# Optimization experiments

Measured on AMD Instinct MI355X. Metric: run time of the kernel, lower is better.

## Reference

```python
import math
import jax, jax.numpy as jnp
import numpy as np

CHANNELS = 256
NUM_HEADS = 4
GROUPS = 32
EPS = 1e-5


def setup_inputs() -> dict:
    key = jax.random.key(0)
    ks = jax.random.split(key, 7)
    b, c, h, w = 8, CHANNELS, 48, 48
    return {
        "x": jax.random.normal(ks[0], (b, c, h, w), dtype=jnp.float32),
        "gn_w": jax.random.uniform(ks[1], (c,), dtype=jnp.float32),
        "gn_b": jax.random.normal(ks[2], (c,), dtype=jnp.float32) * 0.02,
        "qkv_w": jax.random.normal(ks[3], (3 * c, c), dtype=jnp.float32) * (1.0 / math.sqrt(c)),
        "qkv_b": jax.random.normal(ks[4], (3 * c,), dtype=jnp.float32) * 0.02,
        "proj_w": jax.random.normal(ks[5], (c, c), dtype=jnp.float32) * (1.0 / math.sqrt(c)),
        "proj_b": jax.random.normal(ks[6], (c,), dtype=jnp.float32) * 0.02,
    }


def reference(x, gn_w, gn_b, qkv_w, qkv_b, proj_w, proj_b):
    b, c, h, w = x.shape
    nh = NUM_HEADS
    hd = c // nh
    hw = h * w

    # GroupNorm(32, c): normalize over (c/G, h, w) per group
    xg = x.reshape(b, GROUPS, c // GROUPS, h, w)
    mean = jnp.mean(xg, axis=(2, 3, 4), keepdims=True)
    var = jnp.mean(jnp.square(xg - mean), axis=(2, 3, 4), keepdims=True)
    xn = (xg - mean) * jax.lax.rsqrt(var + EPS)
    xn = xn.reshape(b, c, h, w) * gn_w[None, :, None, None] + gn_b[None, :, None, None]

    # 1x1 conv qkv: per-pixel linear
    qkv = jnp.einsum('bchw,oc->bohw', xn, qkv_w) + qkv_b[None, :, None, None]
    q, k, v = jnp.split(qkv, 3, axis=1)  # each (b, c, h, w)

    # split channels into heads: (b, nh, hd, hw)
    q = q.reshape(b, nh, hd, hw)
    k = k.reshape(b, nh, hd, hw)
    v = v.reshape(b, nh, hd, hw)

    scale = 1.0 / math.sqrt(hd)
    attn = jnp.einsum('bndi,bndj->bnij', q, k) * scale  # (b, nh, hw, hw)
    attn = jax.nn.softmax(attn, axis=-1)
    out = jnp.einsum('bnij,bndj->bndi', attn, v)  # (b, nh, hd, hw)
    out = out.reshape(b, c, h, w)

    out = jnp.einsum('bchw,oc->bohw', out, proj_w) + proj_b[None, :, None, None]
    return x + out
```

## Files before the change

kernel.cpp:

```cpp
#include <hip/hip_runtime.h>
#include <hip/hip_bf16.h>
#include <math.h>

#define NB 8
#define NC 256
#define NHW 2304
#define NH 4
#define HD 64
#define CPG 8
#define GN_EPS 1e-5f

typedef __bf16 bf16;
typedef __bf16 bf16x4 __attribute__((ext_vector_type(4)));
typedef __bf16 bf16x8 __attribute__((ext_vector_type(8)));
typedef float f32x4 __attribute__((ext_vector_type(4)));
typedef float f32x16 __attribute__((ext_vector_type(16)));
typedef int i32x4 __attribute__((ext_vector_type(4)));
typedef unsigned int u32;

#define MFMA16(a, b, c) __builtin_amdgcn_mfma_f32_16x16x32_bf16(a, b, c, 0, 0, 0)
#define MFMA32(a, b, c) __builtin_amdgcn_mfma_f32_32x32x16_bf16(a, b, c, 0, 0, 0)

__global__ __launch_bounds__(256) void k_pre(const float* __restrict__ x,
                                             const float* __restrict__ gw,
                                             const float* __restrict__ gb,
                                             const float* __restrict__ qw,
                                             const float* __restrict__ pw,
                                             bf16* __restrict__ xnt,
                                             bf16* __restrict__ wq,
                                             bf16* __restrict__ wp) {
  int t = threadIdx.x;
  if (blockIdx.x < 768) {
    int i = blockIdx.x * 256 + t;
    wq[i] = (bf16)qw[i];
    if (i < NC * NC) wp[i] = (bf16)pw[i];
    return;
  }
  int bid = blockIdx.x - 768;
  int b = bid >> 5;
  int g = bid & 31;
  int c0 = g * CPG;
  const float* xb = x + (b * NC + c0) * NHW;
  float s = 0.f, s2 = 0.f;
  for (int p = t; p < NHW; p += 256) {
#pragma unroll
    for (int cc = 0; cc < CPG; ++cc) {
      float v = xb[cc * NHW + p];
      s += v;
      s2 += v * v;
    }
  }
#pragma unroll
  for (int m = 1; m < 64; m <<= 1) {
    s += __shfl_xor(s, m);
    s2 += __shfl_xor(s2, m);
  }
  __shared__ float red[8];
  int wid = t >> 6;
  if ((t & 63) == 0) { red[wid] = s; red[4 + wid] = s2; }
  __syncthreads();
  s = red[0] + red[1] + red[2] + red[3];
  s2 = red[4] + red[5] + red[6] + red[7];
  const float inv_n = 1.0f / (CPG * NHW);
  float mean = s * inv_n;
  float var = s2 * inv_n - mean * mean;
  float rsq = rsqrtf(var + GN_EPS);
  float ka[CPG], kb[CPG];
#pragma unroll
  for (int cc = 0; cc < CPG; ++cc) {
    float wv = gw[c0 + cc];
    ka[cc] = wv * rsq;
    kb[cc] = gb[c0 + cc] - mean * rsq * wv;
  }
  bf16* dst = xnt + b * NHW * NC + c0;
  for (int p = t; p < NHW; p += 256) {
    bf16x8 o;
#pragma unroll
    for (int cc = 0; cc < CPG; ++cc)
      o[cc] = (bf16)(xb[cc * NHW + p] * ka[cc] + kb[cc]);
    *reinterpret_cast<bf16x8*>(dst + p * NC) = o;
  }
}

__global__ __launch_bounds__(256) void k_qkv(const bf16* __restrict__ xnt,
                                             const bf16* __restrict__ wq,
                                             const float* __restrict__ qkvb,
                                             bf16* __restrict__ qt,
                                             bf16* __restrict__ kt,
                                             bf16* __restrict__ vv) {
  int b = blockIdx.z;
  int i_base = blockIdx.x * 128;
  int o_base = blockIdx.y * 128;
  int t = threadIdx.x;
  int lane = t & 63, wid = t >> 6;
  int wm = (wid >> 1) * 64, wn = (wid & 1) * 64;
  int l15 = lane & 15, g = lane >> 4;
  const bool qk = (o_base < 512);
  const bf16* ab;
  const bf16* bb;
  if (qk) {
    ab = wq + (o_base + wm + l15) * NC + g * 8;
    bb = xnt + ((size_t)b * NHW + i_base + wn + l15) * NC + g * 8;
  } else {
    ab = xnt + ((size_t)b * NHW + i_base + wm + l15) * NC + g * 8;
    bb = wq + (o_base + wn + l15) * NC + g * 8;
  }
  f32x4 acc[4][4] = {};
#pragma unroll 2
  for (int kc = 0; kc < 8; ++kc) {
    bf16x8 af[4], bf[4];
#pragma unroll
    for (int mf = 0; mf < 4; ++mf)
      af[mf] = *reinterpret_cast<const bf16x8*>(ab + mf * 16 * NC + kc * 32);
#pragma unroll
    for (int nf = 0; nf < 4; ++nf)
      bf[nf] = *reinterpret_cast<const bf16x8*>(bb + nf * 16 * NC + kc * 32);
#pragma unroll
    for (int mf = 0; mf < 4; ++mf)
#pragma unroll
      for (int nf = 0; nf < 4; ++nf)
        acc[mf][nf] = MFMA16(af[mf], bf[nf], acc[mf][nf]);
  }
  if (qk) {
    const float qscale = 0.125f * 1.4426950408889634f;
#pragma unroll
    for (int mf = 0; mf < 4; ++mf) {
      int o0 = o_base + wm + mf * 16 + g * 4;
      f32x4 b4 = *reinterpret_cast<const f32x4*>(qkvb + o0);
      bool isQ = (o0 < 256);
      float sc = isQ ? qscale : 1.0f;
      int oo = isQ ? o0 : o0 - 256;
      bf16* base = (isQ ? qt : kt) +
                   ((size_t)(b * NH + (oo >> 6)) * NHW) * HD + (oo & 63);
#pragma unroll
      for (int nf = 0; nf < 4; ++nf) {
        int i = i_base + wn + nf * 16 + l15;
        bf16x4 w;
#pragma unroll
        for (int r = 0; r < 4; ++r)
          w[r] = (bf16)((acc[mf][nf][r] + b4[r]) * sc);
        *reinterpret_cast<bf16x4*>(base + (size_t)i * HD) = w;
      }
    }
  } else {
#pragma unroll
    for (int nf = 0; nf < 4; ++nf) {
      int og = o_base + wn + nf * 16 + l15;
      float bias = qkvb[og];
      int o2 = og - 512;
      bf16* dp = vv + ((size_t)(b * NH + (o2 >> 6)) * HD + (o2 & 63)) * NHW +
                 i_base + wm + g * 4;
#pragma unroll
      for (int mf = 0; mf < 4; ++mf) {
        bf16x4 w;
#pragma unroll
        for (int r = 0; r < 4; ++r) w[r] = (bf16)(acc[mf][nf][r] + bias);
        *reinterpret_cast<bf16x4*>(dp + mf * 16) = w;
      }
    }
  }
}

__global__ __launch_bounds__(256, 4) void k_attn(const bf16* __restrict__ qt,
                                                 const bf16* __restrict__ kt,
                                                 const bf16* __restrict__ vv,
                                                 bf16* __restrict__ att) {
  __shared__ union SM {
    struct { bf16 k[2][4096]; bf16 v[2][4096]; } kv;
    float m[2][64][33];
  } smem;

  const int tid = threadIdx.x;
  const int wid = tid >> 6, lane = tid & 63;
  const int l31 = lane & 31, g2 = lane >> 5;
  const int ig = wid & 1, jsub = wid >> 1;

  const int bid = blockIdx.x;
  const int wg = (bid & 7) * 144 + (bid >> 3);
  const int bh = wg / 36, it = wg % 36;
  const int b = bh >> 2, n = bh & 3;
  const int i0w = it * 64 + ig * 32;

  const bf16* qb = qt + (size_t)bh * NHW * HD;
  const bf16* kb = kt + (size_t)bh * NHW * HD;
  const bf16* vb = vv + (size_t)bh * HD * NHW;

  const int r0 = tid >> 3, cs = tid & 7;
  const bf16* kg0 = kb + r0 * HD + cs * 8;
  const bf16* kg1 = kb + (r0 + 32) * HD + cs * 8;
  const bf16* vg0 = vb + (size_t)r0 * NHW + cs * 8;
  const bf16* vg1 = vb + (size_t)(r0 + 32) * NHW + cs * 8;
#define EOFF(c, row) ((c) * 512 + ((((row) + (c)) & 63) << 3))
  const int lw0 = EOFF(cs, r0);
  const int lw1 = EOFF(cs, r0 + 32);

  int ksw[4];
#pragma unroll
  for (int kk = 0; kk < 4; ++kk) ksw[kk] = EOFF(2 * kk + g2, jsub * 32 + l31);
  int vsw0[2], vsw1[2];
#pragma unroll
  for (int J = 0; J < 2; ++J) {
    int c = jsub * 4 + J * 2 + g2;
    vsw0[J] = EOFF(c, l31);
    vsw1[J] = EOFF(c, l31 + 32);
  }
#undef EOFF

  bf16x8 q[4];
#pragma unroll
  for (int kk = 0; kk < 4; ++kk)
    q[kk] = *reinterpret_cast<const bf16x8*>(qb + (i0w + l31) * HD + kk * 16 + g2 * 8);

  f32x16 acc0 = {}, acc1 = {};
  float l_r = 0.f;

  {
    bf16x8 a = *reinterpret_cast<const bf16x8*>(kg0);
    bf16x8 c = *reinterpret_cast<const bf16x8*>(kg1);
    bf16x8 d = *reinterpret_cast<const bf16x8*>(vg0);
    bf16x8 e = *reinterpret_cast<const bf16x8*>(vg1);
    *reinterpret_cast<bf16x8*>(&smem.kv.k[0][lw0]) = a;
    *reinterpret_cast<bf16x8*>(&smem.kv.k[0][lw1]) = c;
    *reinterpret_cast<bf16x8*>(&smem.kv.v[0][lw0]) = d;
    *reinterpret_cast<bf16x8*>(&smem.kv.v[0][lw1]) = e;
  }
  asm volatile("s_waitcnt lgkmcnt(0)" ::: "memory");
  __builtin_amdgcn_s_barrier();

  for (int t = 0; t < 36; ++t) {
    const int cur = t & 1;
    bf16x8 kr0, kr1, vr0, vr1;
    if (t < 35) {
      kr0 = *reinterpret_cast<const bf16x8*>(kg0 + (t + 1) * (64 * HD));
      kr1 = *reinterpret_cast<const bf16x8*>(kg1 + (t + 1) * (64 * HD));
      vr0 = *reinterpret_cast<const bf16x8*>(vg0 + (t + 1) * 64);
      vr1 = *reinterpret_cast<const bf16x8*>(vg1 + (t + 1) * 64);
    }
    const bf16* kc = smem.kv.k[cur];
    const bf16* vc = smem.kv.v[cur];

    f32x16 s = {};
    __builtin_amdgcn_s_setprio(1);
#pragma unroll
    for (int kk = 0; kk < 4; ++kk) {
      bf16x8 kf = *reinterpret_cast<const bf16x8*>(kc + ksw[kk]);
      s = MFMA32(kf, q[kk], s);
    }
    __builtin_amdgcn_s_setprio(0);

    u32 P[8];
    float la = 0.f, lb = 0.f;
#pragma unroll
    for (int m = 0; m < 8; ++m) {
      float e0 = exp2f(s[2 * m]);
      float e1 = exp2f(s[2 * m + 1]);
      la += e0;
      lb += e1;
      u32 pk;
      asm("v_cvt_pk_bf16_f32 %0, %1, %2" : "=v"(pk) : "v"(e0), "v"(e1));
      P[m] = pk;
    }
    l_r += la + lb;

#pragma unroll
    for (int J = 0; J < 2; ++J) {
      u32 w0 = P[4 * J], w2 = P[4 * J + 2];
      asm("v_permlane32_swap_b32 %0, %1" : "+v"(w0), "+v"(w2));
      u32 w1 = P[4 * J + 1], w3 = P[4 * J + 3];
      asm("v_permlane32_swap_b32 %0, %1" : "+v"(w1), "+v"(w3));
      i32x4 wv;
      wv[0] = (int)w0; wv[1] = (int)w1; wv[2] = (int)w2; wv[3] = (int)w3;
      bf16x8 pf = __builtin_bit_cast(bf16x8, wv);
      bf16x8 v0 = *reinterpret_cast<const bf16x8*>(vc + vsw0[J]);
      bf16x8 v1 = *reinterpret_cast<const bf16x8*>(vc + vsw1[J]);
      __builtin_amdgcn_s_setprio(1);
      acc0 = MFMA32(v0, pf, acc0);
      acc1 = MFMA32(v1, pf, acc1);
      __builtin_amdgcn_s_setprio(0);
    }

    if (t < 35) {
      const int nb = cur ^ 1;
      *reinterpret_cast<bf16x8*>(&smem.kv.k[nb][lw0]) = kr0;
      *reinterpret_cast<bf16x8*>(&smem.kv.k[nb][lw1]) = kr1;
      *reinterpret_cast<bf16x8*>(&smem.kv.v[nb][lw0]) = vr0;
      *reinterpret_cast<bf16x8*>(&smem.kv.v[nb][lw1]) = vr1;
    }
    asm volatile("s_waitcnt lgkmcnt(0)" ::: "memory");
    __builtin_amdgcn_s_barrier();
  }

  if (jsub == 1) {
    float* mb = smem.m[ig][lane];
#pragma unroll
    for (int e = 0; e < 16; ++e) { mb[e] = acc0[e]; mb[16 + e] = acc1[e]; }
    mb[32] = l_r;
  }
  __syncthreads();
  if (jsub == 0) {
    const float* mb = smem.m[ig][lane];
#pragma unroll
    for (int e = 0; e < 16; ++e) { acc0[e] += mb[e]; acc1[e] += mb[16 + e]; }
    l_r += mb[32];
    l_r += __shfl_xor(l_r, 32);
    const float inv = 1.0f / l_r;
    bf16* ob = att + ((size_t)(b * NHW) + i0w + l31) * NC + n * HD;
#pragma unroll
    for (int rq = 0; rq < 4; ++rq) {
      bf16x4 o0, o1;
#pragma unroll
      for (int c = 0; c < 4; ++c) {
        o0[c] = (bf16)(acc0[rq * 4 + c] * inv);
        o1[c] = (bf16)(acc1[rq * 4 + c] * inv);
      }
      *reinterpret_cast<bf16x4*>(ob + 8 * rq + 4 * g2) = o0;
      *reinterpret_cast<bf16x4*>(ob + 32 + 8 * rq + 4 * g2) = o1;
    }
  }
}

__global__ __launch_bounds__(256) void k_proj(const bf16* __restrict__ att,
                                              const bf16* __restrict__ wp,
                                              const float* __restrict__ pb,
                                              const float* __restrict__ x,
                                              float* __restrict__ out) {
  int b = blockIdx.z;
  int i_base = blockIdx.x * 128;
  int o_base = blockIdx.y * 128;
  int t = threadIdx.x;
  int lane = t & 63, wid = t >> 6;
  int wm = (wid >> 1) * 64, wn = (wid & 1) * 64;
  int l15 = lane & 15, g = lane >> 4;
  const bf16* ab = wp + (o_base + wm + l15) * NC + g * 8;
  const bf16* bb = att + (b * NHW + i_base + wn + l15) * NC + g * 8;
  f32x4 acc[4][4] = {};
#pragma unroll 2
  for (int kc = 0; kc < 8; ++kc) {
    bf16x8 af[4], bf[4];
#pragma unroll
    for (int mf = 0; mf < 4; ++mf)
      af[mf] = *reinterpret_cast<const bf16x8*>(ab + mf * 16 * NC + kc * 32);
#pragma unroll
    for (int nf = 0; nf < 4; ++nf)
      bf[nf] = *reinterpret_cast<const bf16x8*>(bb + nf * 16 * NC + kc * 32);
#pragma unroll
    for (int mf = 0; mf < 4; ++mf)
#pragma unroll
      for (int nf = 0; nf < 4; ++nf)
        acc[mf][nf] = MFMA16(af[mf], bf[nf], acc[mf][nf]);
  }
  int orow0 = o_base + wm + g * 4;
#pragma unroll
  for (int mf = 0; mf < 4; ++mf)
#pragma unroll
    for (int r = 0; r < 4; ++r) {
      int o = orow0 + mf * 16 + r;
      float bias = pb[o];
      const float* xr = x + (b * NC + o) * NHW + i_base + wn;
      float* orow = out + (b * NC + o) * NHW + i_base + wn;
#pragma unroll
      for (int nf = 0; nf < 4; ++nf) {
        int i = nf * 16 + l15;
        orow[i] = acc[mf][nf][r] + bias + xr[i];
      }
    }
}

extern "C" void kernel_launch(void* const* d_in, const int* in_sizes, int n_in,
                              void* d_out, int out_size, void* d_ws, size_t ws_size,
                              hipStream_t stream) {
  const float* x    = (const float*)d_in[0];
  const float* gnw  = (const float*)d_in[1];
  const float* gnb  = (const float*)d_in[2];
  const float* qkvw = (const float*)d_in[3];
  const float* qkvb = (const float*)d_in[4];
  const float* pw   = (const float*)d_in[5];
  const float* pb   = (const float*)d_in[6];
  float* out = (float*)d_out;

  bf16* ws = (bf16*)d_ws;
  const size_t NE = (size_t)NB * NHW * NC;
  bf16* xnt = ws;
  bf16* qt  = ws + NE;
  bf16* kt  = ws + 2 * NE;
  bf16* vv  = ws + 3 * NE;
  bf16* att = ws + 4 * NE;
  bf16* wqb = ws + 5 * NE;
  bf16* wpb = wqb + 768 * 256;

  k_pre<<<1024, 256, 0, stream>>>(x, gnw, gnb, qkvw, pw, xnt, wqb, wpb);
  k_qkv<<<dim3(18, 6, NB), 256, 0, stream>>>(xnt, wqb, qkvb, qt, kt, vv);
  k_attn<<<1152, 256, 0, stream>>>(qt, kt, vv, att);
  k_proj<<<dim3(18, 2, NB), 256, 0, stream>>>(att, wpb, pb, x, out);
}
```

Measured before the change: 163.2 us.

## Single-buffer K/V in attention LDS and widen GroupNorm prep blocks

The attention kernel drops LDS double buffering for K/V and uses one buffer, adding a barrier before the next tile is written. This halves K/V shared memory, likely to fit more workgroups per CU, but it serialises the LDS store behind all waves finishing the current tile. Separately, the prep kernel now uses 1024-thread blocks with 16-wave reductions instead of 256-thread blocks, changing the block count and per-block parallelism of the GroupNorm pass.

```diff
diff --git a/kernel.cpp b/kernel.cpp
--- a/kernel.cpp
+++ b/kernel.cpp
@@ -21,28 +21,28 @@
 #define MFMA16(a, b, c) __builtin_amdgcn_mfma_f32_16x16x32_bf16(a, b, c, 0, 0, 0)
 #define MFMA32(a, b, c) __builtin_amdgcn_mfma_f32_32x32x16_bf16(a, b, c, 0, 0, 0)
 
-__global__ __launch_bounds__(256) void k_pre(const float* __restrict__ x,
-                                             const float* __restrict__ gw,
-                                             const float* __restrict__ gb,
-                                             const float* __restrict__ qw,
-                                             const float* __restrict__ pw,
-                                             bf16* __restrict__ xnt,
-                                             bf16* __restrict__ wq,
-                                             bf16* __restrict__ wp) {
+__global__ __launch_bounds__(1024) void k_pre(const float* __restrict__ x,
+                                              const float* __restrict__ gw,
+                                              const float* __restrict__ gb,
+                                              const float* __restrict__ qw,
+                                              const float* __restrict__ pw,
+                                              bf16* __restrict__ xnt,
+                                              bf16* __restrict__ wq,
+                                              bf16* __restrict__ wp) {
   int t = threadIdx.x;
-  if (blockIdx.x < 768) {
-    int i = blockIdx.x * 256 + t;
+  if (blockIdx.x < 192) {
+    int i = blockIdx.x * 1024 + t;
     wq[i] = (bf16)qw[i];
     if (i < NC * NC) wp[i] = (bf16)pw[i];
     return;
   }
-  int bid = blockIdx.x - 768;
+  int bid = blockIdx.x - 192;
   int b = bid >> 5;
   int g = bid & 31;
   int c0 = g * CPG;
   const float* xb = x + (b * NC + c0) * NHW;
   float s = 0.f, s2 = 0.f;
-  for (int p = t; p < NHW; p += 256) {
+  for (int p = t; p < NHW; p += 1024) {
 #pragma unroll
     for (int cc = 0; cc < CPG; ++cc) {
       float v = xb[cc * NHW + p];
@@ -55,12 +55,13 @@
     s += __shfl_xor(s, m);
     s2 += __shfl_xor(s2, m);
   }
-  __shared__ float red[8];
+  __shared__ float red[32];
   int wid = t >> 6;
-  if ((t & 63) == 0) { red[wid] = s; red[4 + wid] = s2; }
+  if ((t & 63) == 0) { red[wid] = s; red[16 + wid] = s2; }
   __syncthreads();
-  s = red[0] + red[1] + red[2] + red[3];
-  s2 = red[4] + red[5] + red[6] + red[7];
+  s = 0.f; s2 = 0.f;
+#pragma unroll
+  for (int w = 0; w < 16; ++w) { s += red[w]; s2 += red[16 + w]; }
   const float inv_n = 1.0f / (CPG * NHW);
   float mean = s * inv_n;
   float var = s2 * inv_n - mean * mean;
@@ -73,7 +74,7 @@
     kb[cc] = gb[c0 + cc] - mean * rsq * wv;
   }
   bf16* dst = xnt + b * NHW * NC + c0;
-  for (int p = t; p < NHW; p += 256) {
+  for (int p = t; p < NHW; p += 1024) {
     bf16x8 o;
 #pragma unroll
     for (int cc = 0; cc < CPG; ++cc)
@@ -166,7 +167,7 @@
                                                  const bf16* __restrict__ vv,
                                                  bf16* __restrict__ att) {
   __shared__ union SM {
-    struct { bf16 k[2][4096]; bf16 v[2][4096]; } kv;
+    struct { bf16 k[4096]; bf16 v[4096]; } kv;
     float m[2][64][33];
   } smem;
 
@@ -219,16 +220,15 @@
     bf16x8 c = *reinterpret_cast<const bf16x8*>(kg1);
     bf16x8 d = *reinterpret_cast<const bf16x8*>(vg0);
     bf16x8 e = *reinterpret_cast<const bf16x8*>(vg1);
-    *reinterpret_cast<bf16x8*>(&smem.kv.k[0][lw0]) = a;
-    *reinterpret_cast<bf16x8*>(&smem.kv.k[0][lw1]) = c;
-    *reinterpret_cast<bf16x8*>(&smem.kv.v[0][lw0]) = d;
-    *reinterpret_cast<bf16x8*>(&smem.kv.v[0][lw1]) = e;
+    *reinterpret_cast<bf16x8*>(&smem.kv.k[lw0]) = a;
+    *reinterpret_cast<bf16x8*>(&smem.kv.k[lw1]) = c;
+    *reinterpret_cast<bf16x8*>(&smem.kv.v[lw0]) = d;
+    *reinterpret_cast<bf16x8*>(&smem.kv.v[lw1]) = e;
   }
   asm volatile("s_waitcnt lgkmcnt(0)" ::: "memory");
   __builtin_amdgcn_s_barrier();
 
   for (int t = 0; t < 36; ++t) {
-    const int cur = t & 1;
     bf16x8 kr0, kr1, vr0, vr1;
     if (t < 35) {
       kr0 = *reinterpret_cast<const bf16x8*>(kg0 + (t + 1) * (64 * HD));
@@ -236,14 +236,12 @@
       vr0 = *reinterpret_cast<const bf16x8*>(vg0 + (t + 1) * 64);
       vr1 = *reinterpret_cast<const bf16x8*>(vg1 + (t + 1) * 64);
     }
-    const bf16* kc = smem.kv.k[cur];
-    const bf16* vc = smem.kv.v[cur];
 
     f32x16 s = {};
     __builtin_amdgcn_s_setprio(1);
 #pragma unroll
     for (int kk = 0; kk < 4; ++kk) {
-      bf16x8 kf = *reinterpret_cast<const bf16x8*>(kc + ksw[kk]);
+      bf16x8 kf = *reinterpret_cast<const bf16x8*>(&smem.kv.k[ksw[kk]]);
       s = MFMA32(kf, q[kk], s);
     }
     __builtin_amdgcn_s_setprio(0);
@@ -271,20 +269,20 @@
       i32x4 wv;
       wv[0] = (int)w0; wv[1] = (int)w1; wv[2] = (int)w2; wv[3] = (int)w3;
       bf16x8 pf = __builtin_bit_cast(bf16x8, wv);
-      bf16x8 v0 = *reinterpret_cast<const bf16x8*>(vc + vsw0[J]);
-      bf16x8 v1 = *reinterpret_cast<const bf16x8*>(vc + vsw1[J]);
+      bf16x8 v0 = *reinterpret_cast<const bf16x8*>(&smem.kv.v[vsw0[J]]);
+      bf16x8 v1 = *reinterpret_cast<const bf16x8*>(&smem.kv.v[vsw1[J]]);
       __builtin_amdgcn_s_setprio(1);
       acc0 = MFMA32(v0, pf, acc0);
       acc1 = MFMA32(v1, pf, acc1);
       __builtin_amdgcn_s_setprio(0);
     }
 
+    __builtin_amdgcn_s_barrier();
     if (t < 35) {
-      const int nb = cur ^ 1;
-      *reinterpret_cast<bf16x8*>(&smem.kv.k[nb][lw0]) = kr0;
-      *reinterpret_cast<bf16x8*>(&smem.kv.k[nb][lw1]) = kr1;
-      *reinterpret_cast<bf16x8*>(&smem.kv.v[nb][lw0]) = vr0;
-      *reinterpret_cast<bf16x8*>(&smem.kv.v[nb][lw1]) = vr1;
+      *reinterpret_cast<bf16x8*>(&smem.kv.k[lw0]) = kr0;
+      *reinterpret_cast<bf16x8*>(&smem.kv.k[lw1]) = kr1;
+      *reinterpret_cast<bf16x8*>(&smem.kv.v[lw0]) = vr0;
+      *reinterpret_cast<bf16x8*>(&smem.kv.v[lw1]) = vr1;
     }
     asm volatile("s_waitcnt lgkmcnt(0)" ::: "memory");
     __builtin_amdgcn_s_barrier();
@@ -388,7 +386,7 @@
   bf16* wqb = ws + 5 * NE;
   bf16* wpb = wqb + 768 * 256;
 
-  k_pre<<<1024, 256, 0, stream>>>(x, gnw, gnb, qkvw, pw, xnt, wqb, wpb);
+  k_pre<<<448, 1024, 0, stream>>>(x, gnw, gnb, qkvw, pw, xnt, wqb, wpb);
   k_qkv<<<dim3(18, 6, NB), 256, 0, stream>>>(xnt, wqb, qkvb, qt, kt, vv);
   k_attn<<<1152, 256, 0, stream>>>(qt, kt, vv, att);
   k_proj<<<dim3(18, 2, NB), 256, 0, stream>>>(att, wpb, pb, x, out);
```

Measured after the change: 208.0 us. +27.4%, slower.
